# Performance work log

Measured on AMD Instinct MI355X. Metric: run time of the kernel, lower is better.

## Reference

```python
import jax, jax.numpy as jnp
import numpy as np

NUM_HEADS = 8


def _conv1x1(x, W, b):
    # 1x1 conv == per-pixel linear: x [N,C,H,W], W [O,C], b [O]
    return jnp.einsum('nchw,oc->nohw', x, W) + b[None, :, None, None]


def setup_inputs() -> dict:
    key = jax.random.key(0)
    ks = jax.random.split(key, 10)
    C = 512
    s = 1.0 / np.sqrt(C)  # keep pre-softmax logits in a sane range
    return {
        'x': jax.random.normal(ks[0], (2, C, 64, 64), dtype=jnp.float32),
        'Wq': jax.random.normal(ks[1], (C, C), dtype=jnp.float32) * s,
        'bq': jax.random.normal(ks[2], (C,), dtype=jnp.float32) * 0.01,
        'Wk': jax.random.normal(ks[3], (C, C), dtype=jnp.float32) * s,
        'bk': jax.random.normal(ks[4], (C,), dtype=jnp.float32) * 0.01,
        'Wv': jax.random.normal(ks[5], (C, C), dtype=jnp.float32) * s,
        'bv': jax.random.normal(ks[6], (C,), dtype=jnp.float32) * 0.01,
        'Wo': jax.random.normal(ks[7], (C, C), dtype=jnp.float32) * s,
        'bo': jax.random.normal(ks[8], (C,), dtype=jnp.float32) * 0.01,
        'gamma': jax.random.normal(ks[9], (1,), dtype=jnp.float32),
    }


def reference(x, Wq, bq, Wk, bk, Wv, bv, Wo, bo, gamma):
    N, C, H, W = x.shape
    nh = NUM_HEADS
    hd = C // nh
    S = H * W
    scale = 1.0 / (hd ** 0.5)
    # Projections via 1x1 conv, then split heads over flattened spatial tokens
    Q = _conv1x1(x, Wq, bq).reshape(N, nh, hd, S).transpose(0, 1, 3, 2)  # [N,h,S,d]
    K = _conv1x1(x, Wk, bk).reshape(N, nh, hd, S)                         # [N,h,d,S]
    V = _conv1x1(x, Wv, bv).reshape(N, nh, hd, S).transpose(0, 1, 3, 2)  # [N,h,S,d]
    attn = jax.nn.softmax(jnp.einsum('nhsd,nhdt->nhst', Q, K) * scale, axis=-1)
    out = jnp.einsum('nhst,nhtd->nhsd', attn, V)                          # [N,h,S,d]
    out = out.transpose(0, 1, 3, 2).reshape(N, C, H, W)
    out = _conv1x1(out, Wo, bo)
    return gamma[0] * out + x
```

## Files before the change

kernel.cpp:

```cpp
#include <hip/hip_runtime.h>
#include <hip/hip_bf16.h>

typedef __attribute__((ext_vector_type(4))) float f32x4;
typedef __attribute__((ext_vector_type(16))) float f32x16;
typedef __attribute__((ext_vector_type(8))) short s16x8;
typedef __attribute__((ext_vector_type(4))) unsigned short us16x4;
typedef __attribute__((ext_vector_type(4))) unsigned int u32x4;

#define C_DIM 512
#define S_DIM 4096
#define NB 2
#define NH 8
#define HD 64

#define QSCALE 0.1803368801111244f

__device__ __forceinline__ unsigned short f2bf(float f) {
    union { float f; unsigned u; } v; v.f = f;
    unsigned r = v.u + 0x7FFFu + ((v.u >> 16) & 1u);
    return (unsigned short)(r >> 16);
}

__device__ __forceinline__ float dev_exp2(float x) {
    float r;
    asm("v_exp_f32 %0, %1" : "=v"(r) : "v"(x));
    return r;
}

__device__ __forceinline__ unsigned cvt_pk_bf16(float lo, float hi) {
    unsigned r;
    asm("v_cvt_pk_bf16_f32 %0, %1, %2" : "=v"(r) : "v"(lo), "v"(hi));
    return r;
}

__device__ __forceinline__ void lane_swap(unsigned& a, unsigned& b) {
    asm("v_permlane32_swap_b32 %0, %1" : "+v"(a), "+v"(b));
}

__device__ __forceinline__ void gload_lds16(const void* g, void* l) {
    __builtin_amdgcn_global_load_lds(
        (const __attribute__((address_space(1))) void*)g,
        (__attribute__((address_space(3))) void*)l, 16, 0, 0);
}

__global__ __launch_bounds__(256) void wconv_kernel(
    const float* __restrict__ Wq, const float* __restrict__ Wk,
    const float* __restrict__ Wv, const float* __restrict__ Wo,
    unsigned short* __restrict__ Wb) {
    int i = blockIdx.x * 256 + threadIdx.x;
    int y = blockIdx.y;
    const float* src = (y == 0) ? Wq : (y == 1) ? Wk : (y == 2) ? Wv : Wo;
    Wb[(size_t)y * 262144 + i] = f2bf(src[i]);
}

__global__ __launch_bounds__(256) void xpose_kernel(
    const float* __restrict__ x, unsigned short* __restrict__ Xt) {
    __shared__ float tile[32][33];
    int n = blockIdx.z;
    int s0 = blockIdx.x * 32;
    int c0 = blockIdx.y * 32;
    int tx = threadIdx.x & 31;
    int ty = threadIdx.x >> 5;
#pragma unroll
    for (int r = 0; r < 4; ++r) {
        int c = c0 + ty + r * 8;
        tile[ty + r * 8][tx] = x[((size_t)n * C_DIM + c) * S_DIM + s0 + tx];
    }
    __syncthreads();
#pragma unroll
    for (int r = 0; r < 4; ++r) {
        int s = s0 + ty + r * 8;
        Xt[((size_t)n * S_DIM + s) * C_DIM + c0 + tx] = f2bf(tile[tx][ty + r * 8]);
    }
}

__global__ __launch_bounds__(256) void qkv_gemm_kernel(
    const unsigned short* __restrict__ Wb, const unsigned short* __restrict__ Xt,
    const float* __restrict__ bq, const float* __restrict__ bk, const float* __restrict__ bv,
    unsigned short* __restrict__ Qt, unsigned short* __restrict__ Kt,
    unsigned short* __restrict__ Vb) {
    __shared__ unsigned short As[128 * 64];
    __shared__ unsigned short Bs[128 * 64];
    int w = blockIdx.z >> 1;
    int n = blockIdx.z & 1;
    const unsigned short* A = Wb + (size_t)w * 262144;
    const unsigned short* B = Xt + (size_t)n * S_DIM * C_DIM;
    int tid = threadIdx.x;
    int wid = tid >> 6, lane = tid & 63;
    int wm = wid >> 1, wn = wid & 1;
    int lr = lane & 15, lq = lane >> 4;
    int bm = blockIdx.y * 128, bt = blockIdx.x * 128;
    int r_in = lane >> 3, c8 = (lane & 7) * 8;

    f32x4 zero = {0.f, 0.f, 0.f, 0.f};
    f32x4 acc[4][4];
#pragma unroll
    for (int i = 0; i < 4; ++i)
#pragma unroll
        for (int j = 0; j < 4; ++j) acc[i][j] = zero;

    for (int ks = 0; ks < 8; ++ks) {
#pragma unroll
        for (int q = 0; q < 4; ++q) {
            int row = wid * 32 + q * 8;
            gload_lds16(A + (size_t)(bm + row + r_in) * C_DIM + ks * 64 + c8, &As[row * 64]);
            gload_lds16(B + (size_t)(bt + row + r_in) * C_DIM + ks * 64 + c8, &Bs[row * 64]);
        }
        __syncthreads();
#pragma unroll
        for (int kk = 0; kk < 2; ++kk) {
            s16x8 af[4], bf[4];
#pragma unroll
            for (int i = 0; i < 4; ++i)
                af[i] = *(const s16x8*)&As[(wm * 64 + i * 16 + lr) * 64 + kk * 32 + lq * 8];
#pragma unroll
            for (int j = 0; j < 4; ++j)
                bf[j] = *(const s16x8*)&Bs[(wn * 64 + j * 16 + lr) * 64 + kk * 32 + lq * 8];
#pragma unroll
            for (int i = 0; i < 4; ++i)
#pragma unroll
                for (int j = 0; j < 4; ++j)
                    acc[i][j] = __builtin_amdgcn_mfma_f32_16x16x32_bf16(af[i], bf[j], acc[i][j], 0, 0, 0);
        }
        __syncthreads();
    }

    const float* bias = (w == 0) ? bq : (w == 1) ? bk : bv;
#pragma unroll
    for (int i = 0; i < 4; ++i) {
        int obase = bm + wm * 64 + i * 16 + lq * 4;
#pragma unroll
        for (int j = 0; j < 4; ++j) {
            int t = bt + wn * 64 + j * 16 + lr;
            if (w == 0) {
                us16x4 pk;
#pragma unroll
                for (int r = 0; r < 4; ++r)
                    pk[r] = f2bf((acc[i][j][r] + bias[obase + r]) * QSCALE);
                int h = obase >> 6, d = obase & 63;
                *(us16x4*)&Qt[(((size_t)(n * NH + h) * S_DIM) + t) * HD + d] = pk;
            } else if (w == 1) {
                us16x4 pk;
#pragma unroll
                for (int r = 0; r < 4; ++r) pk[r] = f2bf(acc[i][j][r] + bias[obase + r]);
                int h = obase >> 6, d = obase & 63;
                *(us16x4*)&Kt[(((size_t)(n * NH + h) * S_DIM) + t) * HD + d] = pk;
            } else {
#pragma unroll
                for (int r = 0; r < 4; ++r) {
                    int o = obase + r;
                    Vb[((size_t)(n * C_DIM + o)) * S_DIM + t] = f2bf(acc[i][j][r] + bias[o]);
                }
            }
        }
    }
}

__global__ __launch_bounds__(256) void attn_kernel(
    const unsigned short* __restrict__ Qt, const unsigned short* __restrict__ Kt,
    const unsigned short* __restrict__ Vb, float* __restrict__ Opart,
    float* __restrict__ Lpart) {
    __shared__ unsigned short Ks[64 * 64];
    __shared__ unsigned short Vs[64 * 64];
    int tid = threadIdx.x, wid = tid >> 6, lane = tid & 63;
    int l31 = lane & 31, hi = lane >> 5;
    int radj = (l31 & 7) ^ ((l31 >> 3) & 3);

    int bidl = blockIdx.x;
    int swz = (bidl & 7) * 128 + (bidl >> 3);
    int nh = swz >> 6;
    int rem = swz & 63;
    int qb = rem >> 1;
    int half = rem & 1;
    int n = nh >> 3, h = nh & 7;
    int qrow0 = qb * 128 + wid * 32;
    int kvbase = half * 2048;

    const unsigned short* Qh = Qt + (size_t)nh * S_DIM * HD;
    const unsigned short* Kh = Kt + (size_t)nh * S_DIM * HD;
    const unsigned short* Vh = Vb + ((size_t)(n * C_DIM + h * HD)) * S_DIM;

    s16x8 qf[4];
#pragma unroll
    for (int st = 0; st < 4; ++st)
        qf[st] = *(const s16x8*)&Qh[((size_t)(qrow0 + l31)) * HD + st * 16 + hi * 8];

    s16x8 ones;
#pragma unroll
    for (int r = 0; r < 8; ++r) ones[r] = (short)0x3F80;

    f32x16 Oacc[2], Lacc;
#pragma unroll
    for (int jm = 0; jm < 2; ++jm)
#pragma unroll
        for (int r = 0; r < 16; ++r) Oacc[jm][r] = 0.f;
#pragma unroll
    for (int r = 0; r < 16; ++r) Lacc[r] = 0.f;

    int srow0 = tid >> 3, sslot = tid & 7;
    int wslot = (sslot ^ (srow0 & 7) ^ ((srow0 >> 3) & 3)) * 8;

    s16x8 kreg[2], vreg[2];
#pragma unroll
    for (int q = 0; q < 2; ++q) {
        int row = srow0 + q * 32;
        kreg[q] = *(const s16x8*)&Kh[((size_t)(kvbase + row)) * HD + sslot * 8];
        vreg[q] = *(const s16x8*)&Vh[((size_t)row) * S_DIM + kvbase + sslot * 8];
    }

    for (int kt = 0; kt < 32; ++kt) {
#pragma unroll
        for (int q = 0; q < 2; ++q) {
            int row = srow0 + q * 32;
            *(s16x8*)&Ks[row * 64 + wslot] = kreg[q];
            *(s16x8*)&Vs[row * 64 + wslot] = vreg[q];
        }
        __syncthreads();
        if (kt < 31) {
#pragma unroll
            for (int q = 0; q < 2; ++q) {
                int row = srow0 + q * 32;
                kreg[q] = *(const s16x8*)&Kh[((size_t)(kvbase + (kt + 1) * 64 + row)) * HD + sslot * 8];
                vreg[q] = *(const s16x8*)&Vh[((size_t)row) * S_DIM + kvbase + (kt + 1) * 64 + sslot * 8];
            }
        }

        f32x16 s_[2];
#pragma unroll
        for (int jm = 0; jm < 2; ++jm) {
#pragma unroll
            for (int r = 0; r < 16; ++r) s_[jm][r] = 0.f;
            int arow = jm * 32 + l31;
#pragma unroll
            for (int st = 0; st < 4; ++st) {
                s16x8 kf = *(const s16x8*)&Ks[arow * 64 + ((2 * st + hi) ^ radj) * 8];
                s_[jm] = __builtin_amdgcn_mfma_f32_32x32x16_bf16(kf, qf[st], s_[jm], 0, 0, 0);
            }
        }

        s16x8 pf[2][2];
#pragma unroll
        for (int jm = 0; jm < 2; ++jm) {
            unsigned pk0 = cvt_pk_bf16(dev_exp2(s_[jm][0]),  dev_exp2(s_[jm][1]));
            unsigned pk1 = cvt_pk_bf16(dev_exp2(s_[jm][2]),  dev_exp2(s_[jm][3]));
            unsigned pk2 = cvt_pk_bf16(dev_exp2(s_[jm][4]),  dev_exp2(s_[jm][5]));
            unsigned pk3 = cvt_pk_bf16(dev_exp2(s_[jm][6]),  dev_exp2(s_[jm][7]));
            unsigned pk4 = cvt_pk_bf16(dev_exp2(s_[jm][8]),  dev_exp2(s_[jm][9]));
            unsigned pk5 = cvt_pk_bf16(dev_exp2(s_[jm][10]), dev_exp2(s_[jm][11]));
            unsigned pk6 = cvt_pk_bf16(dev_exp2(s_[jm][12]), dev_exp2(s_[jm][13]));
            unsigned pk7 = cvt_pk_bf16(dev_exp2(s_[jm][14]), dev_exp2(s_[jm][15]));
            lane_swap(pk2, pk0);
            lane_swap(pk3, pk1);
            lane_swap(pk6, pk4);
            lane_swap(pk7, pk5);
            u32x4 w0 = {pk0, pk1, pk2, pk3};
            u32x4 w1 = {pk4, pk5, pk6, pk7};
            pf[jm][0] = __builtin_bit_cast(s16x8, w0);
            pf[jm][1] = __builtin_bit_cast(s16x8, w1);
        }

#pragma unroll
        for (int jm = 0; jm < 2; ++jm)
#pragma unroll
            for (int st = 0; st < 2; ++st)
                Lacc = __builtin_amdgcn_mfma_f32_32x32x16_bf16(ones, pf[jm][st], Lacc, 0, 0, 0);

#pragma unroll
        for (int jm2 = 0; jm2 < 2; ++jm2) {
            int vrow = jm2 * 32 + l31;
#pragma unroll
            for (int jm = 0; jm < 2; ++jm)
#pragma unroll
                for (int st = 0; st < 2; ++st) {
                    s16x8 vf = *(const s16x8*)&Vs[vrow * 64 + ((jm * 4 + st * 2 + hi) ^ radj) * 8];
                    Oacc[jm2] = __builtin_amdgcn_mfma_f32_32x32x16_bf16(vf, pf[jm][st], Oacc[jm2], 0, 0, 0);
                }
        }
        __syncthreads();
    }

    int token = qrow0 + l31;
    float* obase = Opart + (((size_t)(half * 16 + nh) * S_DIM + token) * HD);
#pragma unroll
    for (int jm2 = 0; jm2 < 2; ++jm2)
#pragma unroll
        for (int rq = 0; rq < 4; ++rq) {
            int d = jm2 * 32 + 8 * rq + 4 * hi;
            f32x4 v = {Oacc[jm2][rq * 4 + 0], Oacc[jm2][rq * 4 + 1],
                       Oacc[jm2][rq * 4 + 2], Oacc[jm2][rq * 4 + 3]};
            *(f32x4*)&obase[d] = v;
        }
    if (hi == 0)
        Lpart[(size_t)(half * 16 + nh) * S_DIM + token] = Lacc[0];
}

__global__ __launch_bounds__(256) void combine_kernel(
    const float* __restrict__ Opart, const float* __restrict__ Lpart,
    unsigned short* __restrict__ Ot) {
    int g = blockIdx.x * 256 + threadIdx.x;
    int d4 = (g & 15) * 4;
    int s = (g >> 4) & 4095;
    int nh = g >> 16;
    size_t base0 = ((size_t)nh * S_DIM + s) * HD + d4;
    size_t base1 = base0 + (size_t)16 * S_DIM * HD;
    f32x4 o0 = *(const f32x4*)&Opart[base0];
    f32x4 o1 = *(const f32x4*)&Opart[base1];
    float l = Lpart[(size_t)nh * S_DIM + s] + Lpart[(size_t)(16 + nh) * S_DIM + s];
    float inv = 1.f / l;
    int n = nh >> 3, h = nh & 7;
    us16x4 pk;
#pragma unroll
    for (int r = 0; r < 4; ++r) pk[r] = f2bf((o0[r] + o1[r]) * inv);
    *(us16x4*)&Ot[((size_t)n * S_DIM + s) * C_DIM + h * HD + d4] = pk;
}

__global__ __launch_bounds__(256) void out_gemm_kernel(
    const unsigned short* __restrict__ Wb, const unsigned short* __restrict__ Ot,
    const float* __restrict__ bo, const float* __restrict__ gamma,
    const float* __restrict__ xin, float* __restrict__ out) {
    __shared__ unsigned short As[128 * 64];
    __shared__ unsigned short Bs[128 * 64];
    int n = blockIdx.z;
    const unsigned short* A = Wb + (size_t)3 * 262144;
    const unsigned short* B = Ot + (size_t)n * S_DIM * C_DIM;
    int tid = threadIdx.x;
    int wid = tid >> 6, lane = tid & 63;
    int wm = wid >> 1, wn = wid & 1;
    int lr = lane & 15, lq = lane >> 4;
    int bm = blockIdx.y * 128, bt = blockIdx.x * 128;
    int r_in = lane >> 3, c8 = (lane & 7) * 8;

    f32x4 zero = {0.f, 0.f, 0.f, 0.f};
    f32x4 acc[4][4];
#pragma unroll
    for (int i = 0; i < 4; ++i)
#pragma unroll
        for (int j = 0; j < 4; ++j) acc[i][j] = zero;

    for (int ks = 0; ks < 8; ++ks) {
#pragma unroll
        for (int q = 0; q < 4; ++q) {
            int row = wid * 32 + q * 8;
            gload_lds16(A + (size_t)(bm + row + r_in) * C_DIM + ks * 64 + c8, &As[row * 64]);
            gload_lds16(B + (size_t)(bt + row + r_in) * C_DIM + ks * 64 + c8, &Bs[row * 64]);
        }
        __syncthreads();
#pragma unroll
        for (int kk = 0; kk < 2; ++kk) {
            s16x8 af[4], bf[4];
#pragma unroll
            for (int i = 0; i < 4; ++i)
                af[i] = *(const s16x8*)&As[(wm * 64 + i * 16 + lr) * 64 + kk * 32 + lq * 8];
#pragma unroll
            for (int j = 0; j < 4; ++j)
                bf[j] = *(const s16x8*)&Bs[(wn * 64 + j * 16 + lr) * 64 + kk * 32 + lq * 8];
#pragma unroll
            for (int i = 0; i < 4; ++i)
#pragma unroll
                for (int j = 0; j < 4; ++j)
                    acc[i][j] = __builtin_amdgcn_mfma_f32_16x16x32_bf16(af[i], bf[j], acc[i][j], 0, 0, 0);
        }
        __syncthreads();
    }

    float g = gamma[0];
#pragma unroll
    for (int i = 0; i < 4; ++i) {
        int obase = bm + wm * 64 + i * 16 + lq * 4;
#pragma unroll
        for (int j = 0; j < 4; ++j) {
            int t = bt + wn * 64 + j * 16 + lr;
#pragma unroll
            for (int r = 0; r < 4; ++r) {
                int o = obase + r;
                size_t idx = ((size_t)(n * C_DIM + o)) * S_DIM + t;
                out[idx] = g * (acc[i][j][r] + bo[o]) + xin[idx];
            }
        }
    }
}

extern "C" void kernel_launch(void* const* d_in, const int* in_sizes, int n_in,
                              void* d_out, int out_size, void* d_ws, size_t ws_size,
                              hipStream_t stream) {
    const float* x  = (const float*)d_in[0];
    const float* Wq = (const float*)d_in[1];
    const float* bq = (const float*)d_in[2];
    const float* Wk = (const float*)d_in[3];
    const float* bk = (const float*)d_in[4];
    const float* Wv = (const float*)d_in[5];
    const float* bv = (const float*)d_in[6];
    const float* Wo = (const float*)d_in[7];
    const float* bo = (const float*)d_in[8];
    const float* gamma = (const float*)d_in[9];
    float* out = (float*)d_out;

    char* ws = (char*)d_ws;
    unsigned short* Wb = (unsigned short*)ws;
    unsigned short* Xt = (unsigned short*)(ws + ((size_t)2  << 20));
    unsigned short* Qt = (unsigned short*)(ws + ((size_t)10 << 20));
    unsigned short* Kt = (unsigned short*)(ws + ((size_t)18 << 20));
    unsigned short* Vb = (unsigned short*)(ws + ((size_t)26 << 20));
    unsigned short* Ot = (unsigned short*)(ws + ((size_t)34 << 20));
    float* Opart = (float*)(ws + ((size_t)42 << 20));
    float* Lpart = (float*)(ws + ((size_t)76 << 20));

    wconv_kernel<<<dim3(1024, 4), 256, 0, stream>>>(Wq, Wk, Wv, Wo, Wb);
    xpose_kernel<<<dim3(128, 16, 2), 256, 0, stream>>>(x, Xt);
    qkv_gemm_kernel<<<dim3(32, 4, 6), 256, 0, stream>>>(Wb, Xt, bq, bk, bv, Qt, Kt, Vb);
    attn_kernel<<<1024, 256, 0, stream>>>(Qt, Kt, Vb, Opart, Lpart);
    combine_kernel<<<4096, 256, 0, stream>>>(Opart, Lpart, Ot);
    out_gemm_kernel<<<dim3(32, 4, 2), 256, 0, stream>>>(Wb, Ot, bo, gamma, x, out);
}
```

Baseline: 156.1 us.

## Double-buffer K/V shared tiles in attention and store partial outputs as bf16

The attention kernel now keeps two LDS buffers for K and V. The next tile is written into the alternate buffer after compute, which leaves one barrier per iteration instead of two. The split-KV partial outputs are also stored as bf16 instead of fp32, halving Opart traffic between the attention and combine kernels. This doubles LDS use, which may lower occupancy, and adds rounding error to the unnormalized partial sums.

```diff
diff --git a/kernel.cpp b/kernel.cpp
--- a/kernel.cpp
+++ b/kernel.cpp
@@ -19,6 +19,11 @@
     union { float f; unsigned u; } v; v.f = f;
     unsigned r = v.u + 0x7FFFu + ((v.u >> 16) & 1u);
     return (unsigned short)(r >> 16);
+}
+
+__device__ __forceinline__ float bf2f(unsigned short u) {
+    union { unsigned u; float f; } v; v.u = ((unsigned)u) << 16;
+    return v.f;
 }
 
 __device__ __forceinline__ float dev_exp2(float x) {
@@ -158,10 +163,10 @@
 
 __global__ __launch_bounds__(256) void attn_kernel(
     const unsigned short* __restrict__ Qt, const unsigned short* __restrict__ Kt,
-    const unsigned short* __restrict__ Vb, float* __restrict__ Opart,
+    const unsigned short* __restrict__ Vb, unsigned short* __restrict__ Opart,
     float* __restrict__ Lpart) {
-    __shared__ unsigned short Ks[64 * 64];
-    __shared__ unsigned short Vs[64 * 64];
+    __shared__ unsigned short Ks[2][64 * 64];
+    __shared__ unsigned short Vs[2][64 * 64];
     int tid = threadIdx.x, wid = tid >> 6, lane = tid & 63;
     int l31 = lane & 31, hi = lane >> 5;
     int radj = (l31 & 7) ^ ((l31 >> 3) & 3);
@@ -207,15 +212,16 @@
         kreg[q] = *(const s16x8*)&Kh[((size_t)(kvbase + row)) * HD + sslot * 8];
         vreg[q] = *(const s16x8*)&Vh[((size_t)row) * S_DIM + kvbase + sslot * 8];
     }
+#pragma unroll
+    for (int q = 0; q < 2; ++q) {
+        int row = srow0 + q * 32;
+        *(s16x8*)&Ks[0][row * 64 + wslot] = kreg[q];
+        *(s16x8*)&Vs[0][row * 64 + wslot] = vreg[q];
+    }
+    __syncthreads();
 
     for (int kt = 0; kt < 32; ++kt) {
-#pragma unroll
-        for (int q = 0; q < 2; ++q) {
-            int row = srow0 + q * 32;
-            *(s16x8*)&Ks[row * 64 + wslot] = kreg[q];
-            *(s16x8*)&Vs[row * 64 + wslot] = vreg[q];
-        }
-        __syncthreads();
+        int cur = kt & 1;
         if (kt < 31) {
 #pragma unroll
             for (int q = 0; q < 2; ++q) {
@@ -233,7 +239,7 @@
             int arow = jm * 32 + l31;
 #pragma unroll
             for (int st = 0; st < 4; ++st) {
-                s16x8 kf = *(const s16x8*)&Ks[arow * 64 + ((2 * st + hi) ^ radj) * 8];
+                s16x8 kf = *(const s16x8*)&Ks[cur][arow * 64 + ((2 * st + hi) ^ radj) * 8];
                 s_[jm] = __builtin_amdgcn_mfma_f32_32x32x16_bf16(kf, qf[st], s_[jm], 0, 0, 0);
             }
         }
@@ -272,30 +278,41 @@
             for (int jm = 0; jm < 2; ++jm)
 #pragma unroll
                 for (int st = 0; st < 2; ++st) {
-                    s16x8 vf = *(const s16x8*)&Vs[vrow * 64 + ((jm * 4 + st * 2 + hi) ^ radj) * 8];
+                    s16x8 vf = *(const s16x8*)&Vs[cur][vrow * 64 + ((jm * 4 + st * 2 + hi) ^ radj) * 8];
                     Oacc[jm2] = __builtin_amdgcn_mfma_f32_32x32x16_bf16(vf, pf[jm][st], Oacc[jm2], 0, 0, 0);
                 }
         }
-        __syncthreads();
+
+        if (kt < 31) {
+            int nxt = cur ^ 1;
+#pragma unroll
+            for (int q = 0; q < 2; ++q) {
+                int row = srow0 + q * 32;
+                *(s16x8*)&Ks[nxt][row * 64 + wslot] = kreg[q];
+                *(s16x8*)&Vs[nxt][row * 64 + wslot] = vreg[q];
+            }
+            __syncthreads();
+        }
     }
 
     int token = qrow0 + l31;
-    float* obase = Opart + (((size_t)(half * 16 + nh) * S_DIM + token) * HD);
+    unsigned short* obase = Opart + (((size_t)(half * 16 + nh) * S_DIM + token) * HD);
 #pragma unroll
     for (int jm2 = 0; jm2 < 2; ++jm2)
 #pragma unroll
         for (int rq = 0; rq < 4; ++rq) {
             int d = jm2 * 32 + 8 * rq + 4 * hi;
-            f32x4 v = {Oacc[jm2][rq * 4 + 0], Oacc[jm2][rq * 4 + 1],
-                       Oacc[jm2][rq * 4 + 2], Oacc[jm2][rq * 4 + 3]};
-            *(f32x4*)&obase[d] = v;
+            us16x4 pk;
+#pragma unroll
+            for (int r = 0; r < 4; ++r) pk[r] = f2bf(Oacc[jm2][rq * 4 + r]);
+            *(us16x4*)&obase[d] = pk;
         }
     if (hi == 0)
         Lpart[(size_t)(half * 16 + nh) * S_DIM + token] = Lacc[0];
 }
 
 __global__ __launch_bounds__(256) void combine_kernel(
-    const float* __restrict__ Opart, const float* __restrict__ Lpart,
+    const unsigned short* __restrict__ Opart, const float* __restrict__ Lpart,
     unsigned short* __restrict__ Ot) {
     int g = blockIdx.x * 256 + threadIdx.x;
     int d4 = (g & 15) * 4;
@@ -303,14 +320,14 @@
     int nh = g >> 16;
     size_t base0 = ((size_t)nh * S_DIM + s) * HD + d4;
     size_t base1 = base0 + (size_t)16 * S_DIM * HD;
-    f32x4 o0 = *(const f32x4*)&Opart[base0];
-    f32x4 o1 = *(const f32x4*)&Opart[base1];
+    us16x4 o0 = *(const us16x4*)&Opart[base0];
+    us16x4 o1 = *(const us16x4*)&Opart[base1];
     float l = Lpart[(size_t)nh * S_DIM + s] + Lpart[(size_t)(16 + nh) * S_DIM + s];
     float inv = 1.f / l;
     int n = nh >> 3, h = nh & 7;
     us16x4 pk;
 #pragma unroll
-    for (int r = 0; r < 4; ++r) pk[r] = f2bf((o0[r] + o1[r]) * inv);
+    for (int r = 0; r < 4; ++r) pk[r] = f2bf((bf2f(o0[r]) + bf2f(o1[r])) * inv);
     *(us16x4*)&Ot[((size_t)n * S_DIM + s) * C_DIM + h * HD + d4] = pk;
 }
 
@@ -402,8 +419,8 @@
     unsigned short* Kt = (unsigned short*)(ws + ((size_t)18 << 20));
     unsigned short* Vb = (unsigned short*)(ws + ((size_t)26 << 20));
     unsigned short* Ot = (unsigned short*)(ws + ((size_t)34 << 20));
-    float* Opart = (float*)(ws + ((size_t)42 << 20));
-    float* Lpart = (float*)(ws + ((size_t)76 << 20));
+    unsigned short* Opart = (unsigned short*)(ws + ((size_t)42 << 20));
+    float* Lpart = (float*)(ws + ((size_t)60 << 20));
 
     wconv_kernel<<<dim3(1024, 4), 256, 0, stream>>>(Wq, Wk, Wv, Wo, Wb);
     xpose_kernel<<<dim3(128, 16, 2), 256, 0, stream>>>(x, Xt);
```

Result: no change. 157.5 us (+0.9%).

## Drop split-KV attention and fuse normalization into attention epilogue

Applied to the files above, without the earlier changes.

Each attention block now iterates over the full key/value sequence instead of half, so the fp32 partial outputs and partial row sums no longer need to be written out and merged. The separate combine kernel is removed, and normalization plus the bf16 conversion happen directly in the attention epilogue. This removes a large fp32 round trip through memory and one kernel launch. In exchange the grid halves, which reduces parallelism and the number of blocks available to hide latency.

```diff
diff --git a/kernel.cpp b/kernel.cpp
--- a/kernel.cpp
+++ b/kernel.cpp
@@ -158,8 +158,7 @@
 
 __global__ __launch_bounds__(256) void attn_kernel(
     const unsigned short* __restrict__ Qt, const unsigned short* __restrict__ Kt,
-    const unsigned short* __restrict__ Vb, float* __restrict__ Opart,
-    float* __restrict__ Lpart) {
+    const unsigned short* __restrict__ Vb, unsigned short* __restrict__ Ot) {
     __shared__ unsigned short Ks[64 * 64];
     __shared__ unsigned short Vs[64 * 64];
     int tid = threadIdx.x, wid = tid >> 6, lane = tid & 63;
@@ -167,14 +166,11 @@
     int radj = (l31 & 7) ^ ((l31 >> 3) & 3);
 
     int bidl = blockIdx.x;
-    int swz = (bidl & 7) * 128 + (bidl >> 3);
-    int nh = swz >> 6;
-    int rem = swz & 63;
-    int qb = rem >> 1;
-    int half = rem & 1;
+    int swz = (bidl & 7) * 64 + (bidl >> 3);
+    int nh = swz >> 5;
+    int qb = swz & 31;
     int n = nh >> 3, h = nh & 7;
     int qrow0 = qb * 128 + wid * 32;
-    int kvbase = half * 2048;
 
     const unsigned short* Qh = Qt + (size_t)nh * S_DIM * HD;
     const unsigned short* Kh = Kt + (size_t)nh * S_DIM * HD;
@@ -204,11 +200,11 @@
 #pragma unroll
     for (int q = 0; q < 2; ++q) {
         int row = srow0 + q * 32;
-        kreg[q] = *(const s16x8*)&Kh[((size_t)(kvbase + row)) * HD + sslot * 8];
-        vreg[q] = *(const s16x8*)&Vh[((size_t)row) * S_DIM + kvbase + sslot * 8];
-    }
-
-    for (int kt = 0; kt < 32; ++kt) {
+        kreg[q] = *(const s16x8*)&Kh[((size_t)row) * HD + sslot * 8];
+        vreg[q] = *(const s16x8*)&Vh[((size_t)row) * S_DIM + sslot * 8];
+    }
+
+    for (int kt = 0; kt < 64; ++kt) {
 #pragma unroll
         for (int q = 0; q < 2; ++q) {
             int row = srow0 + q * 32;
@@ -216,12 +212,12 @@
             *(s16x8*)&Vs[row * 64 + wslot] = vreg[q];
         }
         __syncthreads();
-        if (kt < 31) {
+        if (kt < 63) {
 #pragma unroll
             for (int q = 0; q < 2; ++q) {
                 int row = srow0 + q * 32;
-                kreg[q] = *(const s16x8*)&Kh[((size_t)(kvbase + (kt + 1) * 64 + row)) * HD + sslot * 8];
-                vreg[q] = *(const s16x8*)&Vh[((size_t)row) * S_DIM + kvbase + (kt + 1) * 64 + sslot * 8];
+                kreg[q] = *(const s16x8*)&Kh[((size_t)((kt + 1) * 64 + row)) * HD + sslot * 8];
+                vreg[q] = *(const s16x8*)&Vh[((size_t)row) * S_DIM + (kt + 1) * 64 + sslot * 8];
             }
         }
 
@@ -279,39 +275,19 @@
         __syncthreads();
     }
 
+    float inv = 1.f / Lacc[0];
     int token = qrow0 + l31;
-    float* obase = Opart + (((size_t)(half * 16 + nh) * S_DIM + token) * HD);
+    unsigned short* orow = Ot + ((size_t)n * S_DIM + token) * C_DIM + h * HD;
 #pragma unroll
     for (int jm2 = 0; jm2 < 2; ++jm2)
 #pragma unroll
         for (int rq = 0; rq < 4; ++rq) {
             int d = jm2 * 32 + 8 * rq + 4 * hi;
-            f32x4 v = {Oacc[jm2][rq * 4 + 0], Oacc[jm2][rq * 4 + 1],
-                       Oacc[jm2][rq * 4 + 2], Oacc[jm2][rq * 4 + 3]};
-            *(f32x4*)&obase[d] = v;
-        }
-    if (hi == 0)
-        Lpart[(size_t)(half * 16 + nh) * S_DIM + token] = Lacc[0];
-}
-
-__global__ __launch_bounds__(256) void combine_kernel(
-    const float* __restrict__ Opart, const float* __restrict__ Lpart,
-    unsigned short* __restrict__ Ot) {
-    int g = blockIdx.x * 256 + threadIdx.x;
-    int d4 = (g & 15) * 4;
-    int s = (g >> 4) & 4095;
-    int nh = g >> 16;
-    size_t base0 = ((size_t)nh * S_DIM + s) * HD + d4;
-    size_t base1 = base0 + (size_t)16 * S_DIM * HD;
-    f32x4 o0 = *(const f32x4*)&Opart[base0];
-    f32x4 o1 = *(const f32x4*)&Opart[base1];
-    float l = Lpart[(size_t)nh * S_DIM + s] + Lpart[(size_t)(16 + nh) * S_DIM + s];
-    float inv = 1.f / l;
-    int n = nh >> 3, h = nh & 7;
-    us16x4 pk;
-#pragma unroll
-    for (int r = 0; r < 4; ++r) pk[r] = f2bf((o0[r] + o1[r]) * inv);
-    *(us16x4*)&Ot[((size_t)n * S_DIM + s) * C_DIM + h * HD + d4] = pk;
+            us16x4 pk;
+#pragma unroll
+            for (int r = 0; r < 4; ++r) pk[r] = f2bf(Oacc[jm2][rq * 4 + r] * inv);
+            *(us16x4*)&orow[d] = pk;
+        }
 }
 
 __global__ __launch_bounds__(256) void out_gemm_kernel(
@@ -402,13 +378,10 @@
     unsigned short* Kt = (unsigned short*)(ws + ((size_t)18 << 20));
     unsigned short* Vb = (unsigned short*)(ws + ((size_t)26 << 20));
     unsigned short* Ot = (unsigned short*)(ws + ((size_t)34 << 20));
-    float* Opart = (float*)(ws + ((size_t)42 << 20));
-    float* Lpart = (float*)(ws + ((size_t)76 << 20));
 
     wconv_kernel<<<dim3(1024, 4), 256, 0, stream>>>(Wq, Wk, Wv, Wo, Wb);
     xpose_kernel<<<dim3(128, 16, 2), 256, 0, stream>>>(x, Xt);
     qkv_gemm_kernel<<<dim3(32, 4, 6), 256, 0, stream>>>(Wb, Xt, bq, bk, bv, Qt, Kt, Vb);
-    attn_kernel<<<1024, 256, 0, stream>>>(Qt, Kt, Vb, Opart, Lpart);
-    combine_kernel<<<4096, 256, 0, stream>>>(Opart, Lpart, Ot);
+    attn_kernel<<<512, 256, 0, stream>>>(Qt, Kt, Vb, Ot);
     out_gemm_kernel<<<dim3(32, 4, 2), 256, 0, stream>>>(Wb, Ot, bo, gamma, x, out);
 }
```

New measurement: 148.4 us. 4.9% less time.
